# Optimization experiments

Hardware: AMD Instinct MI355X
Metric: run time of the kernel (lower is better)

Reference implementation:

```python
import jax, jax.numpy as jnp
import numpy as np

# RoIAlign config (matches init_kwargs; sampling_ratio is asserted == 1 in the module)
OH, OW = 7, 7
SPATIAL_SCALE = 0.25
ALIGNED = True
N_ROIS = 2048


def setup_inputs() -> dict:
    key = jax.random.key(0)
    k1, k2, k3, k4 = jax.random.split(key, 4)
    B, C, H, W = 4, 256, 200, 336
    feat = jax.random.normal(k1, (B, C, H, W), jnp.float32)
    # boxes in image coordinates (image = feature / spatial_scale)
    img_h, img_w = H / SPATIAL_SCALE, W / SPATIAL_SCALE
    xs = jnp.sort(jax.random.uniform(k2, (N_ROIS, 2), jnp.float32) * img_w, axis=1)
    ys = jnp.sort(jax.random.uniform(k3, (N_ROIS, 2), jnp.float32) * img_h, axis=1)
    rois = jnp.stack([xs[:, 0], ys[:, 0], xs[:, 1], ys[:, 1]], axis=1)  # [N,4] x1,y1,x2,y2
    roi_batch_idx = jax.random.randint(k4, (N_ROIS,), 0, B, jnp.int32)
    return {"featuremaps": feat, "rois": rois, "roi_batch_idx": roi_batch_idx}


def _roi_align(featuremaps, rois, roi_batch_idx):
    B, C, H, W = featuremaps.shape
    N = rois.shape[0]
    off = 0.5 if ALIGNED else 0.0
    x1 = rois[:, 0] * SPATIAL_SCALE - off
    y1 = rois[:, 1] * SPATIAL_SCALE - off
    x2 = rois[:, 2] * SPATIAL_SCALE - off
    y2 = rois[:, 3] * SPATIAL_SCALE - off
    roi_w = x2 - x1
    roi_h = y2 - y1
    if not ALIGNED:  # legacy behaviour clamps rois to min size 1
        roi_w = jnp.maximum(roi_w, 1.0)
        roi_h = jnp.maximum(roi_h, 1.0)
    bin_w = roi_w / OW
    bin_h = roi_h / OH
    # sampling_ratio == 1 -> single sample at each bin center
    x = x1[:, None] + (jnp.arange(OW, dtype=rois.dtype) + 0.5) * bin_w[:, None]  # [N,OW]
    y = y1[:, None] + (jnp.arange(OH, dtype=rois.dtype) + 0.5) * bin_h[:, None]  # [N,OH]
    xg = jnp.broadcast_to(x[:, None, :], (N, OH, OW))
    yg = jnp.broadcast_to(y[:, :, None], (N, OH, OW))
    # samples outside [-1, H]x[-1, W] produce 0 (torch roi_align semantics)
    valid = (yg >= -1.0) & (yg <= H) & (xg >= -1.0) & (xg <= W)
    yc = jnp.clip(yg, 0.0, H - 1.0)
    xc = jnp.clip(xg, 0.0, W - 1.0)
    yl = jnp.floor(yc).astype(jnp.int32)
    xl = jnp.floor(xc).astype(jnp.int32)
    yh = jnp.minimum(yl + 1, H - 1)
    xh = jnp.minimum(xl + 1, W - 1)
    ly = yc - yl
    lx = xc - xl
    hy = 1.0 - ly
    hx = 1.0 - lx
    b = roi_batch_idx[:, None, None]  # [N,1,1]

    def gather(yi, xi):
        # irregular bilinear-corner gather -> [N, OH, OW, C]
        return featuremaps[b, :, yi, xi]

    val = ((hy * hx)[..., None] * gather(yl, xl)
           + (hy * lx)[..., None] * gather(yl, xh)
           + (ly * hx)[..., None] * gather(yh, xl)
           + (ly * lx)[..., None] * gather(yh, xh))
    out = jnp.where(valid[..., None], val, 0.0)
    return jnp.transpose(out, (0, 3, 1, 2))  # [N, C, OH, OW]


def reference(featuremaps, rois, roi_batch_idx):
    # Quantization path is a fake-quant passthrough here (observer disabled,
    # output scale set to input scale), so float math is the reference.
    return _roi_align(featuremaps, rois, roi_batch_idx)
```

## Files before the change

### kernel.cpp

```cpp
#include <hip/hip_runtime.h>
#include <hip/hip_bf16.h>
#include <hip/hip_fp16.h>

constexpr int B_ = 4, C_ = 256, H_ = 200, W_ = 336;
constexpr int OH_ = 7, OW_ = 7;
constexpr float SCALE_ = 0.25f;
constexpr int HW_ = H_ * W_;
constexpr int OHW_ = OH_ * OW_;

typedef float f32x4 __attribute__((ext_vector_type(4)));

__global__ __launch_bounds__(256) void transpose_bchw_bhwc_f16(
    const float* __restrict__ in, __half* __restrict__ out) {
  __shared__ float tile[64][33];
  const int b  = blockIdx.z;
  const int k0 = blockIdx.x * 32;
  const int c0 = blockIdx.y * 64;
  const float* src = in + (size_t)b * C_ * HW_;
  __half2*     dst = (__half2*)(out + (size_t)b * HW_ * C_);
  const int tx = threadIdx.x & 31;
  const int ty = threadIdx.x >> 5;

#pragma unroll
  for (int p = 0; p < 8; ++p) {
    const int c = p * 8 + ty;
    tile[c][tx] = __builtin_nontemporal_load(
        &src[(size_t)(c0 + c) * HW_ + (k0 + tx)]);
  }
  __syncthreads();
#pragma unroll
  for (int q = 0; q < 4; ++q) {
    const int k = q * 8 + ty;
    const __half2 h = __halves2half2(__float2half(tile[2 * tx][k]),
                                     __float2half(tile[2 * tx + 1][k]));
    dst[(size_t)(k0 + k) * (C_ / 2) + (c0 / 2) + tx] = h;
  }
}

__global__ __launch_bounds__(256) void roi_gather_T_f16(
    const __half* __restrict__ featT, const float* __restrict__ rois,
    const int* __restrict__ bidx, float* __restrict__ out) {
  __shared__ float vals[C_ * OHW_];
  __shared__ int   offs[4][OHW_];
  __shared__ float wts[4][OHW_];
  const int n = blockIdx.x;
  const int t = threadIdx.x;

  if (t < OHW_) {
    const int s = t, oh = s / OW_, ow = s - oh * OW_;
    const float x1 = rois[n * 4 + 0] * SCALE_ - 0.5f;
    const float y1 = rois[n * 4 + 1] * SCALE_ - 0.5f;
    const float x2 = rois[n * 4 + 2] * SCALE_ - 0.5f;
    const float y2 = rois[n * 4 + 3] * SCALE_ - 0.5f;
    const float bw = (x2 - x1) * (1.0f / OW_);
    const float bh = (y2 - y1) * (1.0f / OH_);
    const float x = x1 + ((float)ow + 0.5f) * bw;
    const float y = y1 + ((float)oh + 0.5f) * bh;
    const bool valid =
        (y >= -1.0f) & (y <= (float)H_) & (x >= -1.0f) & (x <= (float)W_);
    const float xc = fminf(fmaxf(x, 0.0f), (float)(W_ - 1));
    const float yc = fminf(fmaxf(y, 0.0f), (float)(H_ - 1));
    const int xl = (int)xc, yl = (int)yc;
    const int xh = min(xl + 1, W_ - 1), yh = min(yl + 1, H_ - 1);
    const float lx = xc - (float)xl, ly = yc - (float)yl;
    const float hx = 1.0f - lx, hy = 1.0f - ly;
    const float vm = valid ? 1.0f : 0.0f;
    offs[0][s] = yl * W_ + xl;  wts[0][s] = vm * hy * hx;
    offs[1][s] = yl * W_ + xh;  wts[1][s] = vm * hy * lx;
    offs[2][s] = yh * W_ + xl;  wts[2][s] = vm * ly * hx;
    offs[3][s] = yh * W_ + xh;  wts[3][s] = vm * ly * lx;
  }
  __syncthreads();

  const int b = bidx[n];
  const __half2* fb2 = (const __half2*)(featT + (size_t)b * HW_ * C_);
  const int cp = t & 127;
  const int sh = t >> 7;

#pragma unroll 5
  for (int i = 0; i < 25; ++i) {
    const int s = 2 * i + sh;
    if (s < OHW_) {
      const float w0 = wts[0][s], w1 = wts[1][s];
      const float w2 = wts[2][s], w3 = wts[3][s];
      const __half2 a0 = fb2[(size_t)offs[0][s] * (C_ / 2) + cp];
      const __half2 a1 = fb2[(size_t)offs[1][s] * (C_ / 2) + cp];
      const __half2 a2 = fb2[(size_t)offs[2][s] * (C_ / 2) + cp];
      const __half2 a3 = fb2[(size_t)offs[3][s] * (C_ / 2) + cp];
      const float2 f0 = __half22float2(a0), f1 = __half22float2(a1);
      const float2 f2 = __half22float2(a2), f3 = __half22float2(a3);
      const float vlo = w0 * f0.x + w1 * f1.x + w2 * f2.x + w3 * f3.x;
      const float vhi = w0 * f0.y + w1 * f1.y + w2 * f2.y + w3 * f3.y;
      vals[(2 * cp)     * OHW_ + s] = vlo;
      vals[(2 * cp + 1) * OHW_ + s] = vhi;
    }
  }
  __syncthreads();

  const f32x4* v4 = (const f32x4*)vals;
  float* po = out + (size_t)n * (C_ * OHW_);
#pragma unroll
  for (int p = 0; p < 13; ++p) {
    const int idx = p * 256 + t;
    if (idx < (C_ * OHW_) / 4) {
      __builtin_nontemporal_store(v4[idx], (f32x4*)&po[idx * 4]);
    }
  }
}

__global__ __launch_bounds__(256) void roi_gather_direct(
    const float* __restrict__ feat, const float* __restrict__ rois,
    const int* __restrict__ bidx, float* __restrict__ out) {
  __shared__ float vals[C_ * OHW_];
  const int n = blockIdx.x;
  const int t = threadIdx.x;

  const float x1 = rois[n * 4 + 0] * SCALE_ - 0.5f;
  const float y1 = rois[n * 4 + 1] * SCALE_ - 0.5f;
  const float x2 = rois[n * 4 + 2] * SCALE_ - 0.5f;
  const float y2 = rois[n * 4 + 3] * SCALE_ - 0.5f;
  const float bw = (x2 - x1) * (1.0f / OW_);
  const float bh = (y2 - y1) * (1.0f / OH_);
  const int b = bidx[n];
  const float* fc = feat + ((size_t)b * C_ + t) * HW_;

  for (int s = 0; s < OHW_; ++s) {
    const int oh = s / OW_, ow = s % OW_;
    const float y = y1 + ((float)oh + 0.5f) * bh;
    const float x = x1 + ((float)ow + 0.5f) * bw;
    const bool valid =
        (y >= -1.0f) & (y <= (float)H_) & (x >= -1.0f) & (x <= (float)W_);
    const float yc = fminf(fmaxf(y, 0.0f), (float)(H_ - 1));
    const float xc = fminf(fmaxf(x, 0.0f), (float)(W_ - 1));
    const int yl = (int)yc;
    const int xl = (int)xc;
    const int yh = min(yl + 1, H_ - 1);
    const int xh = min(xl + 1, W_ - 1);
    const float ly = yc - (float)yl, lx = xc - (float)xl;
    const float hy = 1.0f - ly, hx = 1.0f - lx;

    float v = hy * hx * fc[yl * W_ + xl] + hy * lx * fc[yl * W_ + xh] +
              ly * hx * fc[yh * W_ + xl] + ly * lx * fc[yh * W_ + xh];
    vals[t * OHW_ + s] = valid ? v : 0.0f;
  }
  __syncthreads();

  float* po = out + (size_t)n * (C_ * OHW_);
#pragma unroll
  for (int k = 0; k < OHW_; ++k) {
    po[k * C_ + t] = vals[k * C_ + t];
  }
}

extern "C" void kernel_launch(void* const* d_in, const int* in_sizes, int n_in,
                              void* d_out, int out_size, void* d_ws,
                              size_t ws_size, hipStream_t stream) {
  const float* feat = (const float*)d_in[0];
  const float* rois = (const float*)d_in[1];
  const int*   bidx = (const int*)d_in[2];
  float*       out  = (float*)d_out;
  const int nrois = in_sizes[1] / 4;

  const size_t need = (size_t)B_ * HW_ * C_ * sizeof(__half);
  if (ws_size >= need) {
    __half* featT = (__half*)d_ws;
    dim3 tg(HW_ / 32, C_ / 64, B_);
    transpose_bchw_bhwc_f16<<<tg, 256, 0, stream>>>(feat, featT);
    roi_gather_T_f16<<<nrois, 256, 0, stream>>>(featT, rois, bidx, out);
  } else {
    roi_gather_direct<<<nrois, 256, 0, stream>>>(feat, rois, bidx, out);
  }
}
```

Measured before the change: 116.6 us.

## Widen transpose tile with packed half2 LDS and split gather over channel halves

The transpose now converts channel pairs to half2 before writing shared memory, covers 128 channels per block, and writes 16-byte vectorized rows to the NHWC workspace. The ROI gather is split into two blocks per ROI, each handling 128 channels, which halves shared memory per block (about 25 KB instead of 50 KB). This should allow more resident blocks per CU and more parallelism. The cost is that ROI coordinate setup is duplicated across the two blocks.

New measurement: 111.6 us. 1.05x faster.

```diff
diff --git a/kernel.cpp b/kernel.cpp
--- a/kernel.cpp
+++ b/kernel.cpp
@@ -7,44 +7,52 @@
 constexpr float SCALE_ = 0.25f;
 constexpr int HW_ = H_ * W_;
 constexpr int OHW_ = OH_ * OW_;
+constexpr int CH_ = 128;
 
 typedef float f32x4 __attribute__((ext_vector_type(4)));
 
 __global__ __launch_bounds__(256) void transpose_bchw_bhwc_f16(
     const float* __restrict__ in, __half* __restrict__ out) {
-  __shared__ float tile[64][33];
+  __shared__ unsigned int tileu[32][68];
   const int b  = blockIdx.z;
   const int k0 = blockIdx.x * 32;
-  const int c0 = blockIdx.y * 64;
+  const int c0 = blockIdx.y * 128;
   const float* src = in + (size_t)b * C_ * HW_;
-  __half2*     dst = (__half2*)(out + (size_t)b * HW_ * C_);
+  unsigned int* dst = (unsigned int*)(out + (size_t)b * HW_ * C_);
+
   const int tx = threadIdx.x & 31;
-  const int ty = threadIdx.x >> 5;
-
+  const int rp = threadIdx.x >> 5;
 #pragma unroll
-  for (int p = 0; p < 8; ++p) {
-    const int c = p * 8 + ty;
-    tile[c][tx] = __builtin_nontemporal_load(
-        &src[(size_t)(c0 + c) * HW_ + (k0 + tx)]);
+  for (int i = 0; i < 8; ++i) {
+    const int cu = rp * 8 + i;
+    const float a = __builtin_nontemporal_load(
+        &src[(size_t)(c0 + 2 * cu) * HW_ + k0 + tx]);
+    const float c = __builtin_nontemporal_load(
+        &src[(size_t)(c0 + 2 * cu + 1) * HW_ + k0 + tx]);
+    const __half2 h = __halves2half2(__float2half(a), __float2half(c));
+    tileu[tx][cu] = *(const unsigned int*)&h;
   }
   __syncthreads();
+
+  const int q  = threadIdx.x & 15;
+  const int kk = threadIdx.x >> 4;
 #pragma unroll
-  for (int q = 0; q < 4; ++q) {
-    const int k = q * 8 + ty;
-    const __half2 h = __halves2half2(__float2half(tile[2 * tx][k]),
-                                     __float2half(tile[2 * tx + 1][k]));
-    dst[(size_t)(k0 + k) * (C_ / 2) + (c0 / 2) + tx] = h;
+  for (int p = 0; p < 2; ++p) {
+    const int k = kk + p * 16;
+    const uint4 v = *(const uint4*)&tileu[k][4 * q];
+    *(uint4*)&dst[(size_t)(k0 + k) * (C_ / 2) + (c0 / 2) + 4 * q] = v;
   }
 }
 
 __global__ __launch_bounds__(256) void roi_gather_T_f16(
     const __half* __restrict__ featT, const float* __restrict__ rois,
     const int* __restrict__ bidx, float* __restrict__ out) {
-  __shared__ float vals[C_ * OHW_];
+  __shared__ float vals[CH_ * OHW_];
   __shared__ int   offs[4][OHW_];
   __shared__ float wts[4][OHW_];
-  const int n = blockIdx.x;
-  const int t = threadIdx.x;
+  const int n   = blockIdx.x;
+  const int ch0 = blockIdx.y * CH_;
+  const int t   = threadIdx.x;
 
   if (t < OHW_) {
     const int s = t, oh = s / OW_, ow = s - oh * OW_;
@@ -73,13 +81,14 @@
   __syncthreads();
 
   const int b = bidx[n];
-  const __half2* fb2 = (const __half2*)(featT + (size_t)b * HW_ * C_);
-  const int cp = t & 127;
-  const int sh = t >> 7;
+  const __half2* fb2 =
+      (const __half2*)(featT + (size_t)b * HW_ * C_) + (ch0 >> 1);
+  const int cp = t & 63;
+  const int sh = t >> 6;
 
-#pragma unroll 5
-  for (int i = 0; i < 25; ++i) {
-    const int s = 2 * i + sh;
+#pragma unroll 2
+  for (int i = 0; i < 13; ++i) {
+    const int s = 4 * i + sh;
     if (s < OHW_) {
       const float w0 = wts[0][s], w1 = wts[1][s];
       const float w2 = wts[2][s], w3 = wts[3][s];
@@ -89,20 +98,20 @@
       const __half2 a3 = fb2[(size_t)offs[3][s] * (C_ / 2) + cp];
       const float2 f0 = __half22float2(a0), f1 = __half22float2(a1);
       const float2 f2 = __half22float2(a2), f3 = __half22float2(a3);
-      const float vlo = w0 * f0.x + w1 * f1.x + w2 * f2.x + w3 * f3.x;
-      const float vhi = w0 * f0.y + w1 * f1.y + w2 * f2.y + w3 * f3.y;
-      vals[(2 * cp)     * OHW_ + s] = vlo;
-      vals[(2 * cp + 1) * OHW_ + s] = vhi;
+      vals[(2 * cp)     * OHW_ + s] =
+          w0 * f0.x + w1 * f1.x + w2 * f2.x + w3 * f3.x;
+      vals[(2 * cp + 1) * OHW_ + s] =
+          w0 * f0.y + w1 * f1.y + w2 * f2.y + w3 * f3.y;
     }
   }
   __syncthreads();
 
   const f32x4* v4 = (const f32x4*)vals;
-  float* po = out + (size_t)n * (C_ * OHW_);
+  float* po = out + (size_t)n * (C_ * OHW_) + (size_t)ch0 * OHW_;
 #pragma unroll
-  for (int p = 0; p < 13; ++p) {
+  for (int p = 0; p < 7; ++p) {
     const int idx = p * 256 + t;
-    if (idx < (C_ * OHW_) / 4) {
+    if (idx < (CH_ * OHW_) / 4) {
       __builtin_nontemporal_store(v4[idx], (f32x4*)&po[idx * 4]);
     }
   }
@@ -164,9 +173,10 @@
   const size_t need = (size_t)B_ * HW_ * C_ * sizeof(__half);
   if (ws_size >= need) {
     __half* featT = (__half*)d_ws;
-    dim3 tg(HW_ / 32, C_ / 64, B_);
+    dim3 tg(HW_ / 32, C_ / 128, B_);
     transpose_bchw_bhwc_f16<<<tg, 256, 0, stream>>>(feat, featT);
-    roi_gather_T_f16<<<nrois, 256, 0, stream>>>(featT, rois, bidx, out);
+    dim3 gg(nrois, 2, 1);
+    roi_gather_T_f16<<<gg, 256, 0, stream>>>(featT, rois, bidx, out);
   } else {
     roi_gather_direct<<<nrois, 256, 0, stream>>>(feat, rois, bidx, out);
   }
```
